# Performance work log

Measured on AMD Instinct MI355X. Metric: run time of the kernel, lower is better.

Reference implementation:

```python
import jax, jax.numpy as jnp
import numpy as np

K = 7          # involution kernel size
PAD = (K - 1) // 2
C = 256        # channels
GC = 16        # group_channels (hardcoded in module)
G = C // GC    # groups = 16
RED = C // 4   # reduction channels = 64
EPS = 1e-5


def _bn_eval(x, gamma, beta, mean, var):
    # eval-mode BatchNorm2d over channel dim of NCHW
    inv = gamma / jnp.sqrt(var + EPS)
    return x * inv[None, :, None, None] + (beta - mean * inv)[None, :, None, None]


def setup_inputs() -> dict:
    key = jax.random.key(0)
    ks = jax.random.split(key, 12)
    x = jax.random.normal(ks[0], (8, C, 56, 56), dtype=jnp.float32)
    # conv1: 1x1, C -> C/4, no bias (followed by BN+ReLU)
    w1 = jax.random.normal(ks[1], (RED, C), dtype=jnp.float32) * (1.0 / np.sqrt(C))
    bn1_gamma = 1.0 + 0.1 * jax.random.normal(ks[2], (RED,), dtype=jnp.float32)
    bn1_beta = 0.1 * jax.random.normal(ks[3], (RED,), dtype=jnp.float32)
    bn1_mean = 0.1 * jax.random.normal(ks[4], (RED,), dtype=jnp.float32)
    bn1_var = jax.random.uniform(ks[5], (RED,), dtype=jnp.float32, minval=0.5, maxval=1.5)
    # conv2: 1x1, C/4 -> K^2 * groups, with bias, no BN/act
    w2 = jax.random.normal(ks[6], (K * K * G, RED), dtype=jnp.float32) * (1.0 / np.sqrt(RED))
    b2 = 0.1 * jax.random.normal(ks[7], (K * K * G,), dtype=jnp.float32)
    # final BN on output channels
    bn2_gamma = 1.0 + 0.1 * jax.random.normal(ks[8], (C,), dtype=jnp.float32)
    bn2_beta = 0.1 * jax.random.normal(ks[9], (C,), dtype=jnp.float32)
    bn2_mean = 0.1 * jax.random.normal(ks[10], (C,), dtype=jnp.float32)
    bn2_var = jax.random.uniform(ks[11], (C,), dtype=jnp.float32, minval=0.5, maxval=1.5)
    return {
        "x": x, "w1": w1,
        "bn1_gamma": bn1_gamma, "bn1_beta": bn1_beta, "bn1_mean": bn1_mean, "bn1_var": bn1_var,
        "w2": w2, "b2": b2,
        "bn2_gamma": bn2_gamma, "bn2_beta": bn2_beta, "bn2_mean": bn2_mean, "bn2_var": bn2_var,
    }


def reference(x, w1, bn1_gamma, bn1_beta, bn1_mean, bn1_var,
              w2, b2, bn2_gamma, bn2_beta, bn2_mean, bn2_var):
    b, c, h, w = x.shape
    # --- kernel generation branch (stride == 1, no avgpool) ---
    t = jnp.einsum('bchw,oc->bohw', x, w1)            # [b, RED, h, w]
    t = jax.nn.relu(_bn_eval(t, bn1_gamma, bn1_beta, bn1_mean, bn1_var))
    wgt = jnp.einsum('bchw,oc->bohw', t, w2) + b2[None, :, None, None]  # [b, K^2*G, h, w]
    wgt = wgt.reshape(b, G, K * K, h, w)
    # --- unfold: patches ordered (c, kh, kw) to match nn.Unfold ---
    xp = jnp.pad(x, ((0, 0), (0, 0), (PAD, PAD), (PAD, PAD)))
    patches = jnp.stack(
        [xp[:, :, i:i + h, j:j + w] for i in range(K) for j in range(K)],
        axis=2,
    )  # [b, c, K^2, h, w]
    patches = patches.reshape(b, G, GC, K * K, h, w)
    # --- per-pixel multiply-sum over kernel footprint ---
    out = jnp.einsum('bgkhw,bgckhw->bgchw', wgt, patches).reshape(b, c, h, w)
    out = jax.nn.relu(_bn_eval(out, bn2_gamma, bn2_beta, bn2_mean, bn2_var))
    return out
```

## Files before the change

### kernel.cpp

```cpp
#include <hip/hip_runtime.h>
#include <hip/hip_fp16.h>

#define NB   8
#define NC   256
#define HW   56
#define NPX  3136
#define RED  64
#define NG   16
#define GC   16
#define KS   7
#define KK   49
#define PADK 3
#define XPH  62
#define XPW  64
#define XPSLICE (XPH * XPW)
#define TPX  224
#define NT2  14
#define XT2_CS 644
#define WSTR2  232

typedef float f32x4 __attribute__((ext_vector_type(4)));
typedef _Float16 h16x4 __attribute__((ext_vector_type(4)));
typedef _Float16 h16x8 __attribute__((ext_vector_type(8)));

__global__ __launch_bounds__(256) void prep_kernel(
    const float* __restrict__ x, const float* __restrict__ w1,
    const float* __restrict__ w2, _Float16* __restrict__ xpad,
    _Float16* __restrict__ w1h, _Float16* __restrict__ w2h) {
    int bid = blockIdx.x;
    if (bid < NB * NC) {
        const float* xs = x + (size_t)bid * NPX;
        _Float16* xd = xpad + (size_t)bid * XPSLICE;
#pragma unroll 4
        for (int e = threadIdx.x; e < XPSLICE; e += 256) {
            int row = e >> 6, col = e & 63;
            int h = row - PADK, w = col - PADK;
            float v = (h >= 0 && h < HW && w >= 0 && w < HW) ? xs[h * HW + w] : 0.0f;
            xd[e] = (_Float16)v;
        }
    } else if (bid < NB * NC + NG) {
        int g = bid - NB * NC;
#pragma unroll 4
        for (int e = threadIdx.x; e < 4096; e += 256) {
            int m = e >> 6, k = e & 63;
            float v = (m < KK) ? w2[((size_t)g * KK + m) * RED + k] : 0.0f;
            w2h[(size_t)g * 4096 + e] = (_Float16)v;
        }
    } else {
#pragma unroll 4
        for (int e = threadIdx.x; e < 64 * 256; e += 256)
            w1h[e] = (_Float16)w1[e];
    }
}

__global__ __launch_bounds__(64) void conv1_kernel(
    const _Float16* __restrict__ xpad, const _Float16* __restrict__ w1h,
    const float* __restrict__ g1, const float* __restrict__ be1,
    const float* __restrict__ mu1, const float* __restrict__ var1,
    _Float16* __restrict__ tT) {
    int lane = threadIdx.x;
    int l15 = lane & 15, l4 = lane >> 4;
    int wgid = blockIdx.x;
    int b  = wgid & 7;
    int nt = wgid >> 3;
    int px = nt * 16 + l15;
    int h = px / HW, w = px % HW;

    const _Float16* xp = xpad + (size_t)b * NC * XPSLICE
                       + (h + PADK) * XPW + (w + PADK);

    f32x4 acc0 = {0,0,0,0}, acc1 = {0,0,0,0}, acc2 = {0,0,0,0}, acc3 = {0,0,0,0};
#pragma unroll
    for (int kk = 0; kk < 8; ++kk) {
        h16x8 bfr;
#pragma unroll
        for (int i = 0; i < 8; ++i)
            bfr[i] = xp[(size_t)(kk * 32 + l4 * 8 + i) * XPSLICE];
#pragma unroll
        for (int mt = 0; mt < 4; ++mt) {
            const _Float16* ap = w1h + (mt * 16 + l15) * NC + kk * 32 + l4 * 8;
            h16x8 a = *(const h16x8*)ap;
            f32x4 c = (mt == 0) ? acc0 : (mt == 1) ? acc1 : (mt == 2) ? acc2 : acc3;
            c = __builtin_amdgcn_mfma_f32_16x16x32_f16(a, bfr, c, 0, 0, 0);
            if (mt == 0) acc0 = c; else if (mt == 1) acc1 = c;
            else if (mt == 2) acc2 = c; else acc3 = c;
        }
    }

    _Float16* tb = tT + ((size_t)b * NPX + px) * RED;
#pragma unroll
    for (int mt = 0; mt < 4; ++mt) {
        f32x4 a = (mt == 0) ? acc0 : (mt == 1) ? acc1 : (mt == 2) ? acc2 : acc3;
        int o0 = mt * 16 + l4 * 4;
        h16x4 pk;
#pragma unroll
        for (int r = 0; r < 4; ++r) {
            int o = o0 + r;
            float inv = g1[o] * rsqrtf(var1[o] + 1e-5f);
            float v = a[r] * inv + (be1[o] - mu1[o] * inv);
            pk[r] = (_Float16)fmaxf(v, 0.0f);
        }
        *(h16x4*)(tb + o0) = pk;
    }
}

__global__ __launch_bounds__(448, 3) void involution_kernel(
    const _Float16* __restrict__ xpad, const _Float16* __restrict__ tT,
    const _Float16* __restrict__ w2h, const float* __restrict__ b2,
    const float* __restrict__ g2, const float* __restrict__ be2,
    const float* __restrict__ mu2, const float* __restrict__ var2,
    float* __restrict__ out) {
    __shared__ __align__(16) _Float16 xtap[GC * XT2_CS];
    __shared__ __align__(16) _Float16 wls[KK * WSTR2];

    int tid  = threadIdx.x;
    int lane = tid & 63;
    int wv   = __builtin_amdgcn_readfirstlane(tid >> 6);
    int wgid = blockIdx.x;
    int swz  = (wgid & 7) * 224 + (wgid >> 3);
    int b    = swz / 224;
    int rem  = swz % 224;
    int g    = rem / NT2;
    int tile = rem % NT2;
    int px0 = tile * TPX;
    int R0  = tile * 4;

    const _Float16* xpg = xpad + ((size_t)b * NC + (size_t)g * GC) * XPSLICE;

    h16x8 xr[3];
#pragma unroll
    for (int u = 0; u < 3; ++u) {
        int cid = u * 448 + tid;
        if (cid < 1280) {
            int ch = cid / 80;
            int rm = cid % 80;
            int rr = rm >> 3, c8 = rm & 7;
            xr[u] = *(const h16x8*)(xpg + (size_t)ch * XPSLICE
                                    + (R0 + rr) * XPW + c8 * 8);
        }
    }

    {
        int l15 = lane & 15, l4 = lane >> 4;
        const _Float16* wA = w2h + (size_t)g * 4096;
        const float* bg = b2 + (size_t)g * KK;
        h16x8 a0[4], a1[4];
#pragma unroll
        for (int mt = 0; mt < 4; ++mt) {
            const _Float16* ap = wA + (mt * 16 + l15) * 64 + l4 * 8;
            a0[mt] = *(const h16x8*)(ap);
            a1[mt] = *(const h16x8*)(ap + 32);
        }
#pragma unroll
        for (int it = 0; it < 2; ++it) {
            int nt = wv * 2 + it;
            int pxc = px0 + nt * 16 + l15;
            const _Float16* tp = tT + ((size_t)b * NPX + pxc) * RED + l4 * 8;
            h16x8 bfr0 = *(const h16x8*)tp;
            h16x8 bfr1 = *(const h16x8*)(tp + 32);

            f32x4 acc0 = {0,0,0,0}, acc1 = {0,0,0,0},
                  acc2 = {0,0,0,0}, acc3 = {0,0,0,0};
#pragma unroll
            for (int mt = 0; mt < 4; ++mt) {
                f32x4 a = (mt == 0) ? acc0 : (mt == 1) ? acc1
                        : (mt == 2) ? acc2 : acc3;
                a = __builtin_amdgcn_mfma_f32_16x16x32_f16(a0[mt], bfr0, a, 0, 0, 0);
                a = __builtin_amdgcn_mfma_f32_16x16x32_f16(a1[mt], bfr1, a, 0, 0, 0);
                if (mt == 0) acc0 = a; else if (mt == 1) acc1 = a;
                else if (mt == 2) acc2 = a; else acc3 = a;
            }
            _Float16* wl = wls + nt * 16 + l15;
#pragma unroll
            for (int mt = 0; mt < 4; ++mt) {
                f32x4 a = (mt == 0) ? acc0 : (mt == 1) ? acc1
                        : (mt == 2) ? acc2 : acc3;
#pragma unroll
                for (int r = 0; r < 4; ++r) {
                    int k = mt * 16 + l4 * 4 + r;
                    if (k < KK) wl[k * WSTR2] = (_Float16)(a[r] + bg[k]);
                }
            }
        }
    }

#pragma unroll
    for (int u = 0; u < 3; ++u) {
        int cid = u * 448 + tid;
        if (cid < 1280) {
            int ch = cid / 80;
            int rm = cid % 80;
            int rr = rm >> 3, c8 = rm & 7;
            *(h16x8*)&xtap[ch * XT2_CS + rr * 64 + c8 * 8] = xr[u];
        }
    }
    __syncthreads();

    int octet = tid >> 4;
    int ch    = tid & 15;
    int lin   = octet * 8;
    int lh    = lin / 56;
    int w0    = lin % 56;

    const _Float16* xb0 = xtap + ch * XT2_CS + lh * 64 + w0;
    float acc[8];
#pragma unroll
    for (int p = 0; p < 8; ++p) acc[p] = 0.0f;

#pragma unroll
    for (int i = 0; i < KS; ++i) {
        h16x8 t0 = *(const h16x8*)(xb0 + i * 64);
        h16x8 t1 = *(const h16x8*)(xb0 + i * 64 + 8);
        float cc[16];
#pragma unroll
        for (int p = 0; p < 8; ++p) { cc[p] = (float)t0[p]; cc[8 + p] = (float)t1[p]; }
#pragma unroll
        for (int j = 0; j < KS; ++j) {
            h16x8 wq = *(const h16x8*)&wls[(i * KS + j) * WSTR2 + lin];
#pragma unroll
            for (int p = 0; p < 8; ++p)
                acc[p] = fmaf((float)wq[p], cc[j + p], acc[p]);
        }
    }

    int c_ = g * GC + ch;
    float inv = g2[c_] * rsqrtf(var2[c_] + 1e-5f);
    float off = be2[c_] - mu2[c_] * inv;
    float* op = out + ((size_t)b * NC + c_) * NPX + px0 + lin;
    f32x4 o0, o1;
#pragma unroll
    for (int p = 0; p < 4; ++p) {
        o0[p] = fmaxf(acc[p] * inv + off, 0.0f);
        o1[p] = fmaxf(acc[4 + p] * inv + off, 0.0f);
    }
    *(f32x4*)(op)     = o0;
    *(f32x4*)(op + 4) = o1;
}

extern "C" void kernel_launch(void* const* d_in, const int* in_sizes, int n_in,
                              void* d_out, int out_size, void* d_ws, size_t ws_size,
                              hipStream_t stream) {
    const float* x    = (const float*)d_in[0];
    const float* w1   = (const float*)d_in[1];
    const float* g1   = (const float*)d_in[2];
    const float* be1  = (const float*)d_in[3];
    const float* mu1  = (const float*)d_in[4];
    const float* var1 = (const float*)d_in[5];
    const float* w2   = (const float*)d_in[6];
    const float* b2   = (const float*)d_in[7];
    const float* g2   = (const float*)d_in[8];
    const float* be2  = (const float*)d_in[9];
    const float* mu2  = (const float*)d_in[10];
    const float* var2 = (const float*)d_in[11];
    float* outp = (float*)d_out;

    _Float16* xpad = (_Float16*)d_ws;
    _Float16* tT   = xpad + (size_t)NB * NC * XPSLICE;
    _Float16* w2h  = tT + (size_t)NB * NPX * RED;
    _Float16* w1h  = w2h + (size_t)NG * 4096;

    prep_kernel<<<NB * NC + NG + 1, 256, 0, stream>>>(x, w1, w2, xpad, w1h, w2h);
    conv1_kernel<<<1568, 64, 0, stream>>>(xpad, w1h, g1, be1, mu1, var1, tT);
    involution_kernel<<<1792, 448, 0, stream>>>(
        xpad, tT, w2h, b2, g2, be2, mu2, var2, outp);
}
```

Before: 64.14 us.

## Split conv2 weight generation out of involution into separate kernel with global buffer

Moves the per-pixel kernel-weight generation (conv2 MFMA) out of the fused involution kernel into its own conv2_kernel, which writes fp16 weights to a global workspace buffer. The stencil kernel then reads its 49 weight vectors directly from global memory instead of LDS, with less shared memory and lower register pressure. The aim is to stop MFMA work from serializing with the stencil work and to raise occupancy. In exchange it adds an extra launch and about 2.5 MB of fp16 weight traffic written and then read back.

```diff
diff --git a/kernel.cpp b/kernel.cpp
--- a/kernel.cpp
+++ b/kernel.cpp
@@ -17,7 +17,6 @@
 #define TPX  224
 #define NT2  14
 #define XT2_CS 644
-#define WSTR2  232
 
 typedef float f32x4 __attribute__((ext_vector_type(4)));
 typedef _Float16 h16x4 __attribute__((ext_vector_type(4)));
@@ -104,18 +103,73 @@
     }
 }
 
-__global__ __launch_bounds__(448, 3) void involution_kernel(
-    const _Float16* __restrict__ xpad, const _Float16* __restrict__ tT,
-    const _Float16* __restrict__ w2h, const float* __restrict__ b2,
+__global__ __launch_bounds__(256) void conv2_kernel(
+    const _Float16* __restrict__ tT, const _Float16* __restrict__ w2h,
+    const float* __restrict__ b2, _Float16* __restrict__ wgt) {
+    __shared__ __align__(16) _Float16 wls[KK * 64];
+
+    int tid  = threadIdx.x;
+    int lane = tid & 63;
+    int wv   = __builtin_amdgcn_readfirstlane(tid >> 6);
+    int wgid = blockIdx.x;
+    int swz  = (wgid & 7) * 784 + (wgid >> 3);
+    int tile = swz % 49;
+    int g    = (swz / 49) & 15;
+    int b    = swz / 784;
+    int px0 = tile * 64;
+
+    int l15 = lane & 15, l4 = lane >> 4;
+    int pxc = px0 + wv * 16 + l15;
+    const _Float16* tp = tT + ((size_t)b * NPX + pxc) * RED + l4 * 8;
+    h16x8 bfr0 = *(const h16x8*)tp;
+    h16x8 bfr1 = *(const h16x8*)(tp + 32);
+
+    const _Float16* wA = w2h + (size_t)g * 4096;
+    const float* bg = b2 + (size_t)g * KK;
+    f32x4 acc0 = {0,0,0,0}, acc1 = {0,0,0,0}, acc2 = {0,0,0,0}, acc3 = {0,0,0,0};
+#pragma unroll
+    for (int mt = 0; mt < 4; ++mt) {
+        const _Float16* ap = wA + (mt * 16 + l15) * 64 + l4 * 8;
+        h16x8 a0 = *(const h16x8*)(ap);
+        h16x8 a1 = *(const h16x8*)(ap + 32);
+        f32x4 a = (mt == 0) ? acc0 : (mt == 1) ? acc1 : (mt == 2) ? acc2 : acc3;
+        a = __builtin_amdgcn_mfma_f32_16x16x32_f16(a0, bfr0, a, 0, 0, 0);
+        a = __builtin_amdgcn_mfma_f32_16x16x32_f16(a1, bfr1, a, 0, 0, 0);
+        if (mt == 0) acc0 = a; else if (mt == 1) acc1 = a;
+        else if (mt == 2) acc2 = a; else acc3 = a;
+    }
+    _Float16* wl = wls + wv * 16 + l15;
+#pragma unroll
+    for (int mt = 0; mt < 4; ++mt) {
+        f32x4 a = (mt == 0) ? acc0 : (mt == 1) ? acc1 : (mt == 2) ? acc2 : acc3;
+#pragma unroll
+        for (int r = 0; r < 4; ++r) {
+            int k = mt * 16 + l4 * 4 + r;
+            if (k < KK) wl[k * 64] = (_Float16)(a[r] + bg[k]);
+        }
+    }
+    __syncthreads();
+
+    _Float16* wg_ = wgt + ((size_t)(b * NG + g) * KK) * NPX + px0;
+#pragma unroll
+    for (int u = 0; u < 2; ++u) {
+        int cid = u * 256 + tid;
+        if (cid < 392) {
+            int k = cid >> 3, c8 = cid & 7;
+            *(h16x8*)(wg_ + (size_t)k * NPX + c8 * 8) =
+                *(const h16x8*)&wls[k * 64 + c8 * 8];
+        }
+    }
+}
+
+__global__ __launch_bounds__(448) void stencil_kernel(
+    const _Float16* __restrict__ xpad, const _Float16* __restrict__ wgt,
     const float* __restrict__ g2, const float* __restrict__ be2,
     const float* __restrict__ mu2, const float* __restrict__ var2,
     float* __restrict__ out) {
     __shared__ __align__(16) _Float16 xtap[GC * XT2_CS];
-    __shared__ __align__(16) _Float16 wls[KK * WSTR2];
 
     int tid  = threadIdx.x;
-    int lane = tid & 63;
-    int wv   = __builtin_amdgcn_readfirstlane(tid >> 6);
     int wgid = blockIdx.x;
     int swz  = (wgid & 7) * 224 + (wgid >> 3);
     int b    = swz / 224;
@@ -127,7 +181,6 @@
 
     const _Float16* xpg = xpad + ((size_t)b * NC + (size_t)g * GC) * XPSLICE;
 
-    h16x8 xr[3];
 #pragma unroll
     for (int u = 0; u < 3; ++u) {
         int cid = u * 448 + tid;
@@ -135,63 +188,8 @@
             int ch = cid / 80;
             int rm = cid % 80;
             int rr = rm >> 3, c8 = rm & 7;
-            xr[u] = *(const h16x8*)(xpg + (size_t)ch * XPSLICE
-                                    + (R0 + rr) * XPW + c8 * 8);
-        }
-    }
-
-    {
-        int l15 = lane & 15, l4 = lane >> 4;
-        const _Float16* wA = w2h + (size_t)g * 4096;
-        const float* bg = b2 + (size_t)g * KK;
-        h16x8 a0[4], a1[4];
-#pragma unroll
-        for (int mt = 0; mt < 4; ++mt) {
-            const _Float16* ap = wA + (mt * 16 + l15) * 64 + l4 * 8;
-            a0[mt] = *(const h16x8*)(ap);
-            a1[mt] = *(const h16x8*)(ap + 32);
-        }
-#pragma unroll
-        for (int it = 0; it < 2; ++it) {
-            int nt = wv * 2 + it;
-            int pxc = px0 + nt * 16 + l15;
-            const _Float16* tp = tT + ((size_t)b * NPX + pxc) * RED + l4 * 8;
-            h16x8 bfr0 = *(const h16x8*)tp;
-            h16x8 bfr1 = *(const h16x8*)(tp + 32);
-
-            f32x4 acc0 = {0,0,0,0}, acc1 = {0,0,0,0},
-                  acc2 = {0,0,0,0}, acc3 = {0,0,0,0};
-#pragma unroll
-            for (int mt = 0; mt < 4; ++mt) {
-                f32x4 a = (mt == 0) ? acc0 : (mt == 1) ? acc1
-                        : (mt == 2) ? acc2 : acc3;
-                a = __builtin_amdgcn_mfma_f32_16x16x32_f16(a0[mt], bfr0, a, 0, 0, 0);
-                a = __builtin_amdgcn_mfma_f32_16x16x32_f16(a1[mt], bfr1, a, 0, 0, 0);
-                if (mt == 0) acc0 = a; else if (mt == 1) acc1 = a;
-                else if (mt == 2) acc2 = a; else acc3 = a;
-            }
-            _Float16* wl = wls + nt * 16 + l15;
-#pragma unroll
-            for (int mt = 0; mt < 4; ++mt) {
-                f32x4 a = (mt == 0) ? acc0 : (mt == 1) ? acc1
-                        : (mt == 2) ? acc2 : acc3;
-#pragma unroll
-                for (int r = 0; r < 4; ++r) {
-                    int k = mt * 16 + l4 * 4 + r;
-                    if (k < KK) wl[k * WSTR2] = (_Float16)(a[r] + bg[k]);
-                }
-            }
-        }
-    }
-
-#pragma unroll
-    for (int u = 0; u < 3; ++u) {
-        int cid = u * 448 + tid;
-        if (cid < 1280) {
-            int ch = cid / 80;
-            int rm = cid % 80;
-            int rr = rm >> 3, c8 = rm & 7;
-            *(h16x8*)&xtap[ch * XT2_CS + rr * 64 + c8 * 8] = xr[u];
+            *(h16x8*)&xtap[ch * XT2_CS + rr * 64 + c8 * 8] =
+                *(const h16x8*)(xpg + (size_t)ch * XPSLICE + (R0 + rr) * XPW + c8 * 8);
         }
     }
     __syncthreads();
@@ -203,12 +201,18 @@
     int w0    = lin % 56;
 
     const _Float16* xb0 = xtap + ch * XT2_CS + lh * 64 + w0;
+    const _Float16* wq0 = wgt + ((size_t)(b * NG + g) * KK) * NPX + px0 + lin;
+
     float acc[8];
 #pragma unroll
     for (int p = 0; p < 8; ++p) acc[p] = 0.0f;
 
 #pragma unroll
     for (int i = 0; i < KS; ++i) {
+        h16x8 wq7[KS];
+#pragma unroll
+        for (int j = 0; j < KS; ++j)
+            wq7[j] = *(const h16x8*)(wq0 + (size_t)(i * KS + j) * NPX);
         h16x8 t0 = *(const h16x8*)(xb0 + i * 64);
         h16x8 t1 = *(const h16x8*)(xb0 + i * 64 + 8);
         float cc[16];
@@ -216,10 +220,9 @@
         for (int p = 0; p < 8; ++p) { cc[p] = (float)t0[p]; cc[8 + p] = (float)t1[p]; }
 #pragma unroll
         for (int j = 0; j < KS; ++j) {
-            h16x8 wq = *(const h16x8*)&wls[(i * KS + j) * WSTR2 + lin];
 #pragma unroll
             for (int p = 0; p < 8; ++p)
-                acc[p] = fmaf((float)wq[p], cc[j + p], acc[p]);
+                acc[p] = fmaf((float)wq7[j][p], cc[j + p], acc[p]);
         }
     }
 
@@ -256,11 +259,13 @@
 
     _Float16* xpad = (_Float16*)d_ws;
     _Float16* tT   = xpad + (size_t)NB * NC * XPSLICE;
-    _Float16* w2h  = tT + (size_t)NB * NPX * RED;
+    _Float16* wgt  = tT + (size_t)NB * NPX * RED;
+    _Float16* w2h  = wgt + (size_t)NB * NG * KK * NPX;
     _Float16* w1h  = w2h + (size_t)NG * 4096;
 
     prep_kernel<<<NB * NC + NG + 1, 256, 0, stream>>>(x, w1, w2, xpad, w1h, w2h);
     conv1_kernel<<<1568, 64, 0, stream>>>(xpad, w1h, g1, be1, mu1, var1, tT);
-    involution_kernel<<<1792, 448, 0, stream>>>(
-        xpad, tT, w2h, b2, g2, be2, mu2, var2, outp);
-}
+    conv2_kernel<<<6272, 256, 0, stream>>>(tT, w2h, b2, wgt);
+    stencil_kernel<<<1792, 448, 0, stream>>>(
+        xpad, wgt, g2, be2, mu2, var2, outp);
+}
```

Measured after the change: 85.78 us. 33.7% more time.

## Drop padded fp16 copy of x; read fp32 input directly with in-kernel padding

Applied to the files above, without the earlier changes.

Removes the prep pass that wrote a zero-padded half-precision copy of the whole input tensor. conv1 and the involution kernel now read fp32 x directly, converting to fp16 in registers and handling the border padding with bounds checks and unaligned vector loads. This drops a full write and reread of a large intermediate. In exchange the later kernels read twice as many bytes per element and take extra branches on edge columns.

```diff
diff --git a/kernel.cpp b/kernel.cpp
--- a/kernel.cpp
+++ b/kernel.cpp
@@ -11,35 +11,22 @@
 #define KS   7
 #define KK   49
 #define PADK 3
-#define XPH  62
-#define XPW  64
-#define XPSLICE (XPH * XPW)
 #define TPX  224
 #define NT2  14
 #define XT2_CS 644
 #define WSTR2  232
 
 typedef float f32x4 __attribute__((ext_vector_type(4)));
+typedef float f32x4u __attribute__((ext_vector_type(4), aligned(4)));
 typedef _Float16 h16x4 __attribute__((ext_vector_type(4)));
 typedef _Float16 h16x8 __attribute__((ext_vector_type(8)));
 
 __global__ __launch_bounds__(256) void prep_kernel(
-    const float* __restrict__ x, const float* __restrict__ w1,
-    const float* __restrict__ w2, _Float16* __restrict__ xpad,
+    const float* __restrict__ w1, const float* __restrict__ w2,
     _Float16* __restrict__ w1h, _Float16* __restrict__ w2h) {
     int bid = blockIdx.x;
-    if (bid < NB * NC) {
-        const float* xs = x + (size_t)bid * NPX;
-        _Float16* xd = xpad + (size_t)bid * XPSLICE;
-#pragma unroll 4
-        for (int e = threadIdx.x; e < XPSLICE; e += 256) {
-            int row = e >> 6, col = e & 63;
-            int h = row - PADK, w = col - PADK;
-            float v = (h >= 0 && h < HW && w >= 0 && w < HW) ? xs[h * HW + w] : 0.0f;
-            xd[e] = (_Float16)v;
-        }
-    } else if (bid < NB * NC + NG) {
-        int g = bid - NB * NC;
+    if (bid < NG) {
+        int g = bid;
 #pragma unroll 4
         for (int e = threadIdx.x; e < 4096; e += 256) {
             int m = e >> 6, k = e & 63;
@@ -54,7 +41,7 @@
 }
 
 __global__ __launch_bounds__(64) void conv1_kernel(
-    const _Float16* __restrict__ xpad, const _Float16* __restrict__ w1h,
+    const float* __restrict__ x, const _Float16* __restrict__ w1h,
     const float* __restrict__ g1, const float* __restrict__ be1,
     const float* __restrict__ mu1, const float* __restrict__ var1,
     _Float16* __restrict__ tT) {
@@ -64,10 +51,8 @@
     int b  = wgid & 7;
     int nt = wgid >> 3;
     int px = nt * 16 + l15;
-    int h = px / HW, w = px % HW;
-
-    const _Float16* xp = xpad + (size_t)b * NC * XPSLICE
-                       + (h + PADK) * XPW + (w + PADK);
+
+    const float* xp = x + (size_t)b * NC * NPX + px;
 
     f32x4 acc0 = {0,0,0,0}, acc1 = {0,0,0,0}, acc2 = {0,0,0,0}, acc3 = {0,0,0,0};
 #pragma unroll
@@ -75,7 +60,7 @@
         h16x8 bfr;
 #pragma unroll
         for (int i = 0; i < 8; ++i)
-            bfr[i] = xp[(size_t)(kk * 32 + l4 * 8 + i) * XPSLICE];
+            bfr[i] = (_Float16)xp[(size_t)(kk * 32 + l4 * 8 + i) * NPX];
 #pragma unroll
         for (int mt = 0; mt < 4; ++mt) {
             const _Float16* ap = w1h + (mt * 16 + l15) * NC + kk * 32 + l4 * 8;
@@ -105,7 +90,7 @@
 }
 
 __global__ __launch_bounds__(448, 3) void involution_kernel(
-    const _Float16* __restrict__ xpad, const _Float16* __restrict__ tT,
+    const float* __restrict__ x, const _Float16* __restrict__ tT,
     const _Float16* __restrict__ w2h, const float* __restrict__ b2,
     const float* __restrict__ g2, const float* __restrict__ be2,
     const float* __restrict__ mu2, const float* __restrict__ var2,
@@ -125,7 +110,7 @@
     int px0 = tile * TPX;
     int R0  = tile * 4;
 
-    const _Float16* xpg = xpad + ((size_t)b * NC + (size_t)g * GC) * XPSLICE;
+    const float* xg = x + ((size_t)b * NC + (size_t)g * GC) * NPX;
 
     h16x8 xr[3];
 #pragma unroll
@@ -135,8 +120,33 @@
             int ch = cid / 80;
             int rm = cid % 80;
             int rr = rm >> 3, c8 = rm & 7;
-            xr[u] = *(const h16x8*)(xpg + (size_t)ch * XPSLICE
-                                    + (R0 + rr) * XPW + c8 * 8);
+            int hrow = R0 + rr - PADK;
+            h16x8 v;
+#pragma unroll
+            for (int p = 0; p < 8; ++p) v[p] = (_Float16)0.0f;
+            if (hrow >= 0 && hrow < HW) {
+                const float* xrow = xg + (size_t)ch * NPX + hrow * HW;
+                if (c8 == 0) {
+                    f32x4 a = *(const f32x4*)(xrow);
+                    float a4 = xrow[4];
+                    v[3] = (_Float16)a[0]; v[4] = (_Float16)a[1];
+                    v[5] = (_Float16)a[2]; v[6] = (_Float16)a[3];
+                    v[7] = (_Float16)a4;
+                } else if (c8 == 7) {
+                    f32x4 a = *(const f32x4u*)(xrow + 52);
+                    v[0] = (_Float16)a[1]; v[1] = (_Float16)a[2];
+                    v[2] = (_Float16)a[3];
+                } else {
+                    int w0 = c8 * 8 - 3;
+                    f32x4 a = *(const f32x4u*)(xrow + w0);
+                    f32x4 b4 = *(const f32x4u*)(xrow + w0 + 4);
+                    v[0] = (_Float16)a[0];  v[1] = (_Float16)a[1];
+                    v[2] = (_Float16)a[2];  v[3] = (_Float16)a[3];
+                    v[4] = (_Float16)b4[0]; v[5] = (_Float16)b4[1];
+                    v[6] = (_Float16)b4[2]; v[7] = (_Float16)b4[3];
+                }
+            }
+            xr[u] = v;
         }
     }
 
@@ -254,13 +264,12 @@
     const float* var2 = (const float*)d_in[11];
     float* outp = (float*)d_out;
 
-    _Float16* xpad = (_Float16*)d_ws;
-    _Float16* tT   = xpad + (size_t)NB * NC * XPSLICE;
-    _Float16* w2h  = tT + (size_t)NB * NPX * RED;
-    _Float16* w1h  = w2h + (size_t)NG * 4096;
-
-    prep_kernel<<<NB * NC + NG + 1, 256, 0, stream>>>(x, w1, w2, xpad, w1h, w2h);
-    conv1_kernel<<<1568, 64, 0, stream>>>(xpad, w1h, g1, be1, mu1, var1, tT);
+    _Float16* tT  = (_Float16*)d_ws;
+    _Float16* w2h = tT + (size_t)NB * NPX * RED;
+    _Float16* w1h = w2h + (size_t)NG * 4096;
+
+    prep_kernel<<<NG + 1, 256, 0, stream>>>(w1, w2, w1h, w2h);
+    conv1_kernel<<<1568, 64, 0, stream>>>(x, w1h, g1, be1, mu1, var1, tT);
     involution_kernel<<<1792, 448, 0, stream>>>(
-        xpad, tT, w2h, b2, g2, be2, mu2, var2, outp);
-}
+        x, tT, w2h, b2, g2, be2, mu2, var2, outp);
+}
```

Measured after the change: 64.91 us. About the same (+1.2%).
